# Kernel optimization log

Measured on AMD Instinct MI355X. Metric: run time of the kernel, lower is better.

## Reference

```python
import jax, jax.numpy as jnp
import numpy as np

MIN_LEVEL, MAX_LEVEL = 2, 5

# pywt Wavelet('db4') analysis filters (dec_lo / dec_hi)
DEC_LO = np.array([-0.010597401784997278, 0.032883011666982945, 0.030841381835986965,
                   -0.18703481171888114, -0.02798376941698385, 0.6308807679295904,
                   0.7148465705525415, 0.23037781330885523])
DEC_HI = np.array([-0.23037781330885523, 0.7148465705525415, -0.6308807679295904,
                   -0.02798376941698385, 0.18703481171888114, 0.030841381835986965,
                   -0.032883011666982945, -0.010597401784997278])
# pytorch_wavelets time-reverses the filters and uses cross-correlation (F.conv),
# which is exactly what lax.conv_general_dilated computes.
H0 = jnp.asarray(DEC_LO[::-1].copy(), jnp.float32)
H1 = jnp.asarray(DEC_HI[::-1].copy(), jnp.float32)


def _afb1d(x):
    """One-level analysis filter bank, 'zero' padding mode (pytorch_wavelets afb1d).
    x: (N, 1, T) -> (lo, hi) each (N, 1, floor((T+L-1)/2))."""
    T = x.shape[-1]
    L = H0.shape[0]
    out = (T + L - 1) // 2          # pywt.dwt_coeff_len(T, L, 'zero')
    p = 2 * out - T                 # total pad; extra zero goes to the right if odd
    xp = jnp.pad(x, ((0, 0), (0, 0), (p // 2, p - p // 2)))
    k = jnp.stack([H0, H1])[:, None, :]          # (2, 1, L)
    lohi = jax.lax.conv_general_dilated(
        xp, k, window_strides=(2,), padding='VALID',
        dimension_numbers=('NCH', 'OIH', 'NCH'))
    return lohi[:, 0:1, :], lohi[:, 1:2, :]


def _decompose(x, levels):
    """Batched multi-level DWT cascade over all features at once; per-feature
    decomposition level selected afterwards via one-hot / masking (same math as
    the original per-feature Python loop)."""
    B, S, F = x.shape
    cur = jnp.transpose(x, (0, 2, 1)).reshape(B * F, 1, S)
    los, his = [], []
    for _ in range(MAX_LEVEL):
        lo, hi = _afb1d(cur)

        def to_bsf(a):
            # zero-pad coeffs up to seq_len, back to (B, S, F) layout
            a = jnp.pad(a, ((0, 0), (0, 0), (0, S - a.shape[-1])))
            return jnp.transpose(a.reshape(B, F, S), (0, 2, 1))

        los.append(to_bsf(lo))
        his.append(to_bsf(hi))
        cur = lo
    los = jnp.stack(los)   # (MAX_LEVEL, B, S, F) lowpass after level j+1
    his = jnp.stack(his)   # (MAX_LEVEL, B, S, F) detail at level j+1

    # approx for feature f = lowpass after `levels[f]` levels
    sel = jax.nn.one_hot(levels - 1, MAX_LEVEL, dtype=x.dtype)      # (F, MAX_LEVEL)
    approx = jnp.einsum('lbsf,fl->bsf', los, sel)
    # details[i] only populated for i < levels[f]
    mask = (jnp.arange(MAX_LEVEL)[:, None] < levels[None, :]).astype(x.dtype)  # (L, F)
    details = his * mask[:, None, None, :]
    high_freq = details.sum(axis=0)
    low_freq = approx
    return approx, details, high_freq, low_freq


def setup_inputs() -> dict:
    key = jax.random.key(0)
    k1, k2 = jax.random.split(key)
    x = jax.random.normal(k1, (32, 4096, 64), jnp.float32)
    complexity_scores = jax.random.uniform(k2, (64,), jnp.float32)
    return {"x": x, "complexity_scores": complexity_scores}


def reference(x, complexity_scores):
    # level_scaled = min_level + round(score * (max_level - min_level)); Python round
    # and jnp.round both use round-half-to-even.
    levels = MIN_LEVEL + jnp.round(
        complexity_scores * (MAX_LEVEL - MIN_LEVEL)).astype(jnp.int32)
    levels = jnp.clip(levels, MIN_LEVEL, MAX_LEVEL)   # (F,)
    return _decompose(x, levels)
```

## Files before the change

### kernel.cpp

```cpp
#include <hip/hip_runtime.h>


#define NB 32
#define NS 4096
#define NF 64
#define BSF (NB * NS * NF)
#define NF4 (NF / 4)

typedef float f4v __attribute__((ext_vector_type(4)));

__constant__ float c_h0[8] = {
     0.23037781330885523f,  0.7148465705525415f,   0.6308807679295904f,
    -0.02798376941698385f, -0.18703481171888114f,  0.030841381835986965f,
     0.032883011666982945f, -0.010597401784997278f};
__constant__ float c_h1[8] = {
    -0.010597401784997278f, -0.032883011666982945f, 0.030841381835986965f,
     0.18703481171888114f,  -0.02798376941698385f,  -0.6308807679295904f,
     0.7148465705525415f,   -0.23037781330885523f};

__device__ __forceinline__ int get_level(const float* __restrict__ scores, int f) {
    int lv = 2 + (int)rintf(scores[f] * 3.0f);
    return min(5, max(2, lv));
}

template <int J, int TIN, int LOG2LEN>
__global__ __launch_bounds__(256) void wl_lvl(
    const f4v* __restrict__ in, f4v* __restrict__ lo_out,
    f4v* __restrict__ det, const float* __restrict__ scores)
{
    constexpr int LEN = 1 << LOG2LEN;
    int t = blockIdx.x * 256 + threadIdx.x;
    int f4 = t & (NF4 - 1);
    int r = t >> 4;
    int n = r & (LEN - 1);
    int b = r >> LOG2LEN;

    const f4v* row = in + (size_t)b * TIN * NF4 + f4;
    const f4v z = {0.f, 0.f, 0.f, 0.f};
    int base = 2 * n - 3;
    f4v lo = z, hi = z;
#pragma unroll
    for (int i = 0; i < 8; ++i) {
        int m = base + i;
        if ((unsigned)m < (unsigned)TIN) {
            f4v v = row[(size_t)m * NF4];
            lo += c_h0[i] * v;
            hi += c_h1[i] * v;
        }
    }
    if (J >= 3) {
        int f0 = f4 * 4;
#pragma unroll
        for (int c = 0; c < 4; ++c)
            if (get_level(scores, f0 + c) < J) hi[c] = 0.f;
    }
    lo_out[(size_t)(b * LEN + n) * NF4 + f4] = lo;
    det[(size_t)(b * NS + n) * NF4 + f4] = hi;
}

__global__ __launch_bounds__(256) void wl_final(
    const float* __restrict__ lo2s, const float* __restrict__ lo3s,
    const float* __restrict__ lo4s, f4v* __restrict__ out4,
    const float* __restrict__ scores)
{
    const int SZA = NB * 1024 * NF4;
    const int SZ5 = NB * 128 * NF4;
    const int SZH = NB * 2048 * NF4;
    int t = blockIdx.x * 256 + threadIdx.x;

    const f4v z = {0.f, 0.f, 0.f, 0.f};
    f4v* det1 = out4 + (size_t)1 * (BSF / 4);
    f4v* det2 = out4 + (size_t)2 * (BSF / 4);
    f4v* det3 = out4 + (size_t)3 * (BSF / 4);
    f4v* det4 = out4 + (size_t)4 * (BSF / 4);
    f4v* det5 = out4 + (size_t)5 * (BSF / 4);
    f4v* high = out4 + (size_t)6 * (BSF / 4);
    f4v* low  = out4 + (size_t)7 * (BSF / 4);
    const f4v* lo4v = (const f4v*)lo4s;

    if (t < SZA) {
        int f4 = t & (NF4 - 1);
        int r = t >> 4;
        int n = r & 1023;
        int b = r >> 10;
        int f0 = f4 * 4;
        int lv[4];
#pragma unroll
        for (int c = 0; c < 4; ++c) lv[c] = get_level(scores, f0 + c);

        f4v l5 = z;
        if (n < 128 && (lv[0] == 5 || lv[1] == 5 || lv[2] == 5 || lv[3] == 5)) {
            const f4v* lo4row = lo4v + (size_t)b * 256 * NF4 + f4;
            int base = 2 * n - 3;
#pragma unroll
            for (int i = 0; i < 8; ++i) {
                int m = base + i;
                if ((unsigned)m < 256u) l5 += c_h0[i] * lo4row[(size_t)m * NF4];
            }
        }
        f4v av = z;
#pragma unroll
        for (int c = 0; c < 4; ++c) {
            int L = lv[c];
            int len = 2048 >> (L - 1);
            float vv = 0.f;
            if (n < len) {
                if (L == 5)      vv = l5[c];
                else if (L == 4) vv = lo4s[(size_t)(b * 256 + n) * NF + f0 + c];
                else if (L == 3) vv = lo3s[(size_t)(b * 512 + n) * NF + f0 + c];
                else             vv = lo2s[(size_t)(b * 1024 + n) * NF + f0 + c];
            }
            av[c] = vv;
        }
        size_t o = (size_t)(b * NS + n) * NF4 + f4;
        __builtin_nontemporal_store(av, out4 + o);
        __builtin_nontemporal_store(av, low + o);
        return;
    }
    t -= SZA;

    if (t < SZ5) {
        int f4 = t & (NF4 - 1);
        int r = t >> 4;
        int n = r & 127;
        int b = r >> 7;
        int f0 = f4 * 4;
        const f4v* lo4row = lo4v + (size_t)b * 256 * NF4 + f4;
        int base = 2 * n - 3;
        f4v hi = z;
#pragma unroll
        for (int i = 0; i < 8; ++i) {
            int m = base + i;
            if ((unsigned)m < 256u) hi += c_h1[i] * lo4row[(size_t)m * NF4];
        }
        f4v d5 = z;
#pragma unroll
        for (int c = 0; c < 4; ++c)
            d5[c] = (get_level(scores, f0 + c) >= 5) ? hi[c] : 0.f;
        __builtin_nontemporal_store(d5, det5 + (size_t)(b * NS + n) * NF4 + f4);
        return;
    }
    t -= SZ5;

    if (t < SZH) {
        int f4 = t & (NF4 - 1);
        int r = t >> 4;
        int n = r & 2047;
        int b = r >> 11;
        int f0 = f4 * 4;

        f4v d5 = z;
        if (n < 128) {
            const f4v* lo4row = lo4v + (size_t)b * 256 * NF4 + f4;
            int base = 2 * n - 3;
            f4v hi = z;
#pragma unroll
            for (int i = 0; i < 8; ++i) {
                int m = base + i;
                if ((unsigned)m < 256u) hi += c_h1[i] * lo4row[(size_t)m * NF4];
            }
#pragma unroll
            for (int c = 0; c < 4; ++c)
                d5[c] = (get_level(scores, f0 + c) >= 5) ? hi[c] : 0.f;
        }
        size_t o = (size_t)(b * NS + n) * NF4 + f4;
        f4v acc = d5 + det1[o];
        if (n < 1024) acc += det2[o];
        if (n < 512)  acc += det3[o];
        if (n < 256)  acc += det4[o];
        __builtin_nontemporal_store(acc, high + o);
    }
}

extern "C" void kernel_launch(void* const* d_in, const int* in_sizes, int n_in,
                              void* d_out, int out_size, void* d_ws, size_t ws_size,
                              hipStream_t stream)
{
    const f4v* x        = (const f4v*)d_in[0];
    const float* scores = (const float*)d_in[1];
    f4v* out4 = (f4v*)d_out;
    float* ws = (float*)d_ws;

    f4v* lo1 = (f4v*)ws;
    f4v* lo2 = lo1 + (size_t)NB * 2048 * NF4;
    f4v* lo3 = lo2 + (size_t)NB * 1024 * NF4;
    f4v* lo4 = lo3 + (size_t)NB * 512 * NF4;

    f4v* det1 = out4 + (size_t)1 * (BSF / 4);
    f4v* det2 = out4 + (size_t)2 * (BSF / 4);
    f4v* det3 = out4 + (size_t)3 * (BSF / 4);
    f4v* det4 = out4 + (size_t)4 * (BSF / 4);

    dim3 block(256);
    wl_lvl<1, 4096, 11><<<dim3(4096), block, 0, stream>>>(x,   lo1, det1, scores);
    wl_lvl<2, 2048, 10><<<dim3(2048), block, 0, stream>>>(lo1, lo2, det2, scores);
    wl_lvl<3, 1024,  9><<<dim3(1024), block, 0, stream>>>(lo2, lo3, det3, scores);
    wl_lvl<4,  512,  8><<<dim3( 512), block, 0, stream>>>(lo3, lo4, det4, scores);
    wl_final<<<dim3(6400), block, 0, stream>>>((const float*)lo2, (const float*)lo3,
                                               (const float*)lo4, out4, scores);
}
```

Before: 281.3 us.

## Fuse four DWT cascade levels into one LDS-tiled kernel with halo recompute

Replaces the four per-level kernels with one kernel in which each workgroup owns a time tile of one batch. The block computes the level-1 through level-4 lowpass coefficients into shared memory, recomputing halo rows, and emits the detail bands plus level-5 lo/hi directly. This removes the global write and reread of the large level-1 lowpass buffer and several kernel launches. The level-5 filtering also moves out of the final kernel, which now only gathers the approximation and sums the details. The cost is redundant halo computation, shrinking thread utilisation in the deeper levels, and block-wide barriers.

```diff
diff --git a/kernel.cpp b/kernel.cpp
--- a/kernel.cpp
+++ b/kernel.cpp
@@ -23,60 +23,211 @@
     return min(5, max(2, lv));
 }
 
-template <int J, int TIN, int LOG2LEN>
-__global__ __launch_bounds__(256) void wl_lvl(
-    const f4v* __restrict__ in, f4v* __restrict__ lo_out,
-    f4v* __restrict__ det, const float* __restrict__ scores)
+__global__ __launch_bounds__(256) void wl_mega(
+    const f4v* __restrict__ x, f4v* __restrict__ out4,
+    f4v* __restrict__ ws, const float* __restrict__ scores)
 {
-    constexpr int LEN = 1 << LOG2LEN;
-    int t = blockIdx.x * 256 + threadIdx.x;
-    int f4 = t & (NF4 - 1);
-    int r = t >> 4;
-    int n = r & (LEN - 1);
-    int b = r >> LOG2LEN;
-
-    const f4v* row = in + (size_t)b * TIN * NF4 + f4;
+    __shared__ f4v lds[3840];
+    f4v* const L1 = lds;
+    f4v* const L2 = lds + 2592;
+    f4v* const L3 = lds;
+    f4v* const L4 = lds + 576;
+
+    const int wg = blockIdx.x;
+    const int b  = wg >> 5;
+    const int ts = wg & 31;
+    const int f4 = threadIdx.x & 15;
+    const int rr = threadIdx.x >> 4;
+    const int f0 = f4 * 4;
     const f4v z = {0.f, 0.f, 0.f, 0.f};
-    int base = 2 * n - 3;
-    f4v lo = z, hi = z;
-#pragma unroll
-    for (int i = 0; i < 8; ++i) {
-        int m = base + i;
-        if ((unsigned)m < (unsigned)TIN) {
-            f4v v = row[(size_t)m * NF4];
+
+    const f4v* const xcol = x + (size_t)b * NS * NF4 + f4;
+    f4v* const det1 = out4 + (size_t)1 * (BSF / 4);
+    f4v* const det2 = out4 + (size_t)2 * (BSF / 4);
+    f4v* const det3 = out4 + (size_t)3 * (BSF / 4);
+    f4v* const det4 = out4 + (size_t)4 * (BSF / 4);
+    f4v* const det5 = out4 + (size_t)5 * (BSF / 4);
+    f4v* const lo2w = ws;
+    f4v* const lo3w = lo2w + (size_t)NB * 1024 * NF4;
+    f4v* const lo4w = lo3w + (size_t)NB * 512 * NF4;
+    f4v* const lo5w = lo4w + (size_t)NB * 256 * NF4;
+
+    int lv[4];
+#pragma unroll
+    for (int c = 0; c < 4; ++c) lv[c] = get_level(scores, f0 + c);
+
+    const int a1 = 64 * ts - 45;
+    const int a2 = 32 * ts - 21;
+    const int a3 = 16 * ts - 9;
+    const int a4 = 8 * ts - 3;
+
+#pragma unroll
+    for (int k = 0; k < 11; ++k) {
+        int ro = rr + 16 * k;
+        if (ro < 162) {
+            int m = a1 + ro;
+            if ((unsigned)m < 2048u) {
+                f4v lo = z;
+#pragma unroll
+                for (int i = 0; i < 8; ++i) {
+                    int mm = 2 * m - 3 + i;
+                    if ((unsigned)mm < (unsigned)NS) lo += c_h0[i] * xcol[(size_t)mm * NF4];
+                }
+                L1[ro * 16 + f4] = lo;
+            }
+        }
+    }
+#pragma unroll
+    for (int k = 0; k < 4; ++k) {
+        int n = 64 * ts + rr + 16 * k;
+        f4v hi = z;
+#pragma unroll
+        for (int i = 0; i < 8; ++i) {
+            int mm = 2 * n - 3 + i;
+            if ((unsigned)mm < (unsigned)NS) hi += c_h1[i] * xcol[(size_t)mm * NF4];
+        }
+        det1[(size_t)(b * NS + n) * NF4 + f4] = hi;
+    }
+    __syncthreads();
+
+#pragma unroll
+    for (int k = 0; k < 5; ++k) {
+        int ro = rr + 16 * k;
+        if (ro < 78) {
+            int m = a2 + ro;
+            if ((unsigned)m < 1024u) {
+                f4v lo = z;
+#pragma unroll
+                for (int i = 0; i < 8; ++i) {
+                    int mm = 2 * m - 3 + i;
+                    f4v v = ((unsigned)mm < 2048u) ? L1[(mm - a1) * 16 + f4] : z;
+                    lo += c_h0[i] * v;
+                }
+                L2[ro * 16 + f4] = lo;
+            }
+        }
+    }
+#pragma unroll
+    for (int k = 0; k < 2; ++k) {
+        int n = 32 * ts + rr + 16 * k;
+        f4v hi = z;
+#pragma unroll
+        for (int i = 0; i < 8; ++i) {
+            int mm = 2 * n - 3 + i;
+            f4v v = ((unsigned)mm < 2048u) ? L1[(mm - a1) * 16 + f4] : z;
+            hi += c_h1[i] * v;
+        }
+        det2[(size_t)(b * NS + n) * NF4 + f4] = hi;
+    }
+    __syncthreads();
+
+#pragma unroll
+    for (int k = 0; k < 3; ++k) {
+        int ro = rr + 16 * k;
+        if (ro < 36) {
+            int m = a3 + ro;
+            if ((unsigned)m < 512u) {
+                f4v lo = z;
+#pragma unroll
+                for (int i = 0; i < 8; ++i) {
+                    int mm = 2 * m - 3 + i;
+                    f4v v = ((unsigned)mm < 1024u) ? L2[(mm - a2) * 16 + f4] : z;
+                    lo += c_h0[i] * v;
+                }
+                L3[ro * 16 + f4] = lo;
+            }
+        }
+    }
+    {
+        int n = 16 * ts + rr;
+        f4v hi = z;
+#pragma unroll
+        for (int i = 0; i < 8; ++i) {
+            int mm = 2 * n - 3 + i;
+            f4v v = ((unsigned)mm < 1024u) ? L2[(mm - a2) * 16 + f4] : z;
+            hi += c_h1[i] * v;
+        }
+#pragma unroll
+        for (int c = 0; c < 4; ++c) if (lv[c] < 3) hi[c] = 0.f;
+        det3[(size_t)(b * NS + n) * NF4 + f4] = hi;
+    }
+#pragma unroll
+    for (int k = 0; k < 2; ++k) {
+        int n = 32 * ts + rr + 16 * k;
+        lo2w[(size_t)(b * 1024 + n) * NF4 + f4] = L2[(n - a2) * 16 + f4];
+    }
+    __syncthreads();
+
+    if (rr < 15) {
+        int m = a4 + rr;
+        if ((unsigned)m < 256u) {
+            f4v lo = z;
+#pragma unroll
+            for (int i = 0; i < 8; ++i) {
+                int mm = 2 * m - 3 + i;
+                f4v v = ((unsigned)mm < 512u) ? L3[(mm - a3) * 16 + f4] : z;
+                lo += c_h0[i] * v;
+            }
+            L4[rr * 16 + f4] = lo;
+        }
+    }
+    if (rr < 8) {
+        int n = 8 * ts + rr;
+        f4v hi = z;
+#pragma unroll
+        for (int i = 0; i < 8; ++i) {
+            int mm = 2 * n - 3 + i;
+            f4v v = ((unsigned)mm < 512u) ? L3[(mm - a3) * 16 + f4] : z;
+            hi += c_h1[i] * v;
+        }
+#pragma unroll
+        for (int c = 0; c < 4; ++c) if (lv[c] < 4) hi[c] = 0.f;
+        det4[(size_t)(b * NS + n) * NF4 + f4] = hi;
+    }
+    {
+        int n = 16 * ts + rr;
+        lo3w[(size_t)(b * 512 + n) * NF4 + f4] = L3[(n - a3) * 16 + f4];
+    }
+    __syncthreads();
+
+    if (rr < 8) {
+        int n = 8 * ts + rr;
+        lo4w[(size_t)(b * 256 + n) * NF4 + f4] = L4[(n - a4) * 16 + f4];
+    }
+    if (rr < 4) {
+        int n = 4 * ts + rr;
+        f4v lo = z, hi = z;
+#pragma unroll
+        for (int i = 0; i < 8; ++i) {
+            int mm = 2 * n - 3 + i;
+            f4v v = ((unsigned)mm < 256u) ? L4[(mm - a4) * 16 + f4] : z;
             lo += c_h0[i] * v;
             hi += c_h1[i] * v;
         }
-    }
-    if (J >= 3) {
-        int f0 = f4 * 4;
-#pragma unroll
-        for (int c = 0; c < 4; ++c)
-            if (get_level(scores, f0 + c) < J) hi[c] = 0.f;
-    }
-    lo_out[(size_t)(b * LEN + n) * NF4 + f4] = lo;
-    det[(size_t)(b * NS + n) * NF4 + f4] = hi;
+        lo5w[(size_t)(b * 128 + n) * NF4 + f4] = lo;
+        f4v d5;
+#pragma unroll
+        for (int c = 0; c < 4; ++c) d5[c] = (lv[c] >= 5) ? hi[c] : 0.f;
+        det5[(size_t)(b * NS + n) * NF4 + f4] = d5;
+    }
 }
 
 __global__ __launch_bounds__(256) void wl_final(
     const float* __restrict__ lo2s, const float* __restrict__ lo3s,
-    const float* __restrict__ lo4s, f4v* __restrict__ out4,
-    const float* __restrict__ scores)
+    const float* __restrict__ lo4s, const float* __restrict__ lo5s,
+    f4v* __restrict__ out4, const float* __restrict__ scores)
 {
     const int SZA = NB * 1024 * NF4;
-    const int SZ5 = NB * 128 * NF4;
-    const int SZH = NB * 2048 * NF4;
     int t = blockIdx.x * 256 + threadIdx.x;
 
+    f4v* const det1 = out4 + (size_t)1 * (BSF / 4);
+    f4v* const det2 = out4 + (size_t)2 * (BSF / 4);
+    f4v* const det3 = out4 + (size_t)3 * (BSF / 4);
+    f4v* const det4 = out4 + (size_t)4 * (BSF / 4);
+    f4v* const det5 = out4 + (size_t)5 * (BSF / 4);
+    f4v* const high = out4 + (size_t)6 * (BSF / 4);
+    f4v* const lowp = out4 + (size_t)7 * (BSF / 4);
     const f4v z = {0.f, 0.f, 0.f, 0.f};
-    f4v* det1 = out4 + (size_t)1 * (BSF / 4);
-    f4v* det2 = out4 + (size_t)2 * (BSF / 4);
-    f4v* det3 = out4 + (size_t)3 * (BSF / 4);
-    f4v* det4 = out4 + (size_t)4 * (BSF / 4);
-    f4v* det5 = out4 + (size_t)5 * (BSF / 4);
-    f4v* high = out4 + (size_t)6 * (BSF / 4);
-    f4v* low  = out4 + (size_t)7 * (BSF / 4);
-    const f4v* lo4v = (const f4v*)lo4s;
 
     if (t < SZA) {
         int f4 = t & (NF4 - 1);
@@ -84,90 +235,34 @@
         int n = r & 1023;
         int b = r >> 10;
         int f0 = f4 * 4;
-        int lv[4];
-#pragma unroll
-        for (int c = 0; c < 4; ++c) lv[c] = get_level(scores, f0 + c);
-
-        f4v l5 = z;
-        if (n < 128 && (lv[0] == 5 || lv[1] == 5 || lv[2] == 5 || lv[3] == 5)) {
-            const f4v* lo4row = lo4v + (size_t)b * 256 * NF4 + f4;
-            int base = 2 * n - 3;
-#pragma unroll
-            for (int i = 0; i < 8; ++i) {
-                int m = base + i;
-                if ((unsigned)m < 256u) l5 += c_h0[i] * lo4row[(size_t)m * NF4];
-            }
-        }
         f4v av = z;
 #pragma unroll
         for (int c = 0; c < 4; ++c) {
-            int L = lv[c];
-            int len = 2048 >> (L - 1);
+            int L = get_level(scores, f0 + c);
             float vv = 0.f;
-            if (n < len) {
-                if (L == 5)      vv = l5[c];
-                else if (L == 4) vv = lo4s[(size_t)(b * 256 + n) * NF + f0 + c];
-                else if (L == 3) vv = lo3s[(size_t)(b * 512 + n) * NF + f0 + c];
-                else             vv = lo2s[(size_t)(b * 1024 + n) * NF + f0 + c];
-            }
+            if (L == 2)      vv = lo2s[(size_t)(b * 1024 + n) * NF + f0 + c];
+            else if (L == 3) { if (n < 512) vv = lo3s[(size_t)(b * 512 + n) * NF + f0 + c]; }
+            else if (L == 4) { if (n < 256) vv = lo4s[(size_t)(b * 256 + n) * NF + f0 + c]; }
+            else             { if (n < 128) vv = lo5s[(size_t)(b * 128 + n) * NF + f0 + c]; }
             av[c] = vv;
         }
         size_t o = (size_t)(b * NS + n) * NF4 + f4;
         __builtin_nontemporal_store(av, out4 + o);
-        __builtin_nontemporal_store(av, low + o);
+        __builtin_nontemporal_store(av, lowp + o);
         return;
     }
     t -= SZA;
-
-    if (t < SZ5) {
-        int f4 = t & (NF4 - 1);
-        int r = t >> 4;
-        int n = r & 127;
-        int b = r >> 7;
-        int f0 = f4 * 4;
-        const f4v* lo4row = lo4v + (size_t)b * 256 * NF4 + f4;
-        int base = 2 * n - 3;
-        f4v hi = z;
-#pragma unroll
-        for (int i = 0; i < 8; ++i) {
-            int m = base + i;
-            if ((unsigned)m < 256u) hi += c_h1[i] * lo4row[(size_t)m * NF4];
-        }
-        f4v d5 = z;
-#pragma unroll
-        for (int c = 0; c < 4; ++c)
-            d5[c] = (get_level(scores, f0 + c) >= 5) ? hi[c] : 0.f;
-        __builtin_nontemporal_store(d5, det5 + (size_t)(b * NS + n) * NF4 + f4);
-        return;
-    }
-    t -= SZ5;
-
-    if (t < SZH) {
+    {
         int f4 = t & (NF4 - 1);
         int r = t >> 4;
         int n = r & 2047;
         int b = r >> 11;
-        int f0 = f4 * 4;
-
-        f4v d5 = z;
-        if (n < 128) {
-            const f4v* lo4row = lo4v + (size_t)b * 256 * NF4 + f4;
-            int base = 2 * n - 3;
-            f4v hi = z;
-#pragma unroll
-            for (int i = 0; i < 8; ++i) {
-                int m = base + i;
-                if ((unsigned)m < 256u) hi += c_h1[i] * lo4row[(size_t)m * NF4];
-            }
-#pragma unroll
-            for (int c = 0; c < 4; ++c)
-                d5[c] = (get_level(scores, f0 + c) >= 5) ? hi[c] : 0.f;
-        }
         size_t o = (size_t)(b * NS + n) * NF4 + f4;
-        f4v acc = d5 + det1[o];
+        f4v acc = det1[o];
         if (n < 1024) acc += det2[o];
         if (n < 512)  acc += det3[o];
         if (n < 256)  acc += det4[o];
+        if (n < 128)  acc += det5[o];
         __builtin_nontemporal_store(acc, high + o);
     }
 }
@@ -179,23 +274,15 @@
     const f4v* x        = (const f4v*)d_in[0];
     const float* scores = (const float*)d_in[1];
     f4v* out4 = (f4v*)d_out;
-    float* ws = (float*)d_ws;
-
-    f4v* lo1 = (f4v*)ws;
-    f4v* lo2 = lo1 + (size_t)NB * 2048 * NF4;
-    f4v* lo3 = lo2 + (size_t)NB * 1024 * NF4;
-    f4v* lo4 = lo3 + (size_t)NB * 512 * NF4;
-
-    f4v* det1 = out4 + (size_t)1 * (BSF / 4);
-    f4v* det2 = out4 + (size_t)2 * (BSF / 4);
-    f4v* det3 = out4 + (size_t)3 * (BSF / 4);
-    f4v* det4 = out4 + (size_t)4 * (BSF / 4);
+    f4v* ws   = (f4v*)d_ws;
+
+    const float* lo2s = (const float*)ws;
+    const float* lo3s = lo2s + (size_t)NB * 1024 * NF;
+    const float* lo4s = lo3s + (size_t)NB * 512 * NF;
+    const float* lo5s = lo4s + (size_t)NB * 256 * NF;
 
     dim3 block(256);
-    wl_lvl<1, 4096, 11><<<dim3(4096), block, 0, stream>>>(x,   lo1, det1, scores);
-    wl_lvl<2, 2048, 10><<<dim3(2048), block, 0, stream>>>(lo1, lo2, det2, scores);
-    wl_lvl<3, 1024,  9><<<dim3(1024), block, 0, stream>>>(lo2, lo3, det3, scores);
-    wl_lvl<4,  512,  8><<<dim3( 512), block, 0, stream>>>(lo3, lo4, det4, scores);
-    wl_final<<<dim3(6400), block, 0, stream>>>((const float*)lo2, (const float*)lo3,
-                                               (const float*)lo4, out4, scores);
-}
+    wl_mega<<<dim3(NB * 32), block, 0, stream>>>(x, out4, ws, scores);
+    wl_final<<<dim3((NB * 1024 * NF4 + NB * 2048 * NF4) / 256), block, 0, stream>>>(
+        lo2s, lo3s, lo4s, lo5s, out4, scores);
+}
```

Measured after the change: 303.8 us. 8.0% more time.
